# Optimization experiments

Hardware: AMD Instinct MI355X
Metric: run time of the kernel (lower is better)

The kernel has to match this reference:

```python
import jax, jax.numpy as jnp
import numpy as np
from jax import lax

T, X, H = 16384, 256, 1024
A_SCALE, A_IDENT = 0.1, 0.9


def setup_inputs() -> dict:
    key = jax.random.key(0)
    k1, k2, k3 = jax.random.split(key, 3)
    x_seq = jax.random.normal(k1, (T, X), dtype=jnp.float32)
    h0 = jnp.zeros((H,), dtype=jnp.float32)
    # orthogonal-like init for A_raw (QR of a gaussian), lecun_normal for B
    g = jax.random.normal(k2, (H, H), dtype=jnp.float32)
    A_raw, _ = jnp.linalg.qr(g)
    B = jax.random.normal(k3, (H, X), dtype=jnp.float32) * (1.0 / np.sqrt(X))
    c = jnp.zeros((H,), dtype=jnp.float32)
    return {"x_seq": x_seq, "h0": h0, "A_raw": A_raw, "B": B, "c": c}


def reference(x_seq, h0, A_raw, B, c):
    # A = a_identity * I + a_scale * A_raw  (computed in setup(), a parameter transform)
    A = A_IDENT * jnp.eye(H, dtype=x_seq.dtype) + A_SCALE * A_raw
    # Precompute input projections for all timesteps as one GEMM: (T,H)
    Bx_c = x_seq @ B.T + c  # B @ x_t + c for every t

    def step(h, bx_t):
        h_new = jnp.tanh(A @ h + bx_t)
        return h_new, h_new

    _, h_all = lax.scan(step, h0, Bx_c)
    return h_all  # (T, H)
```

## Files before the change

kernel.cpp:

```cpp
#include <hip/hip_runtime.h>
#include <cstdint>

#define T_LEN 16384
#define X_DIM 256
#define H_DIM 1024
#define NREP  8
#define SLOT_U32 1024
#define REP_U32  (2 * SLOT_U32)
#define FLAG_OFF (NREP * REP_U32)

typedef unsigned int u32;
typedef u32   u32x4 __attribute__((ext_vector_type(4)));
typedef float f32x4 __attribute__((ext_vector_type(4)));

__device__ __forceinline__ void coh_store4(u32* p, u32x4 v) {
  asm volatile("global_store_dwordx4 %0, %1, off sc0 sc1" :: "v"(p), "v"(v) : "memory");
}
__device__ __forceinline__ void coh_store1(u32* p, u32 v) {
  asm volatile("global_store_dword %0, %1, off sc0 sc1" :: "v"(p), "v"(v) : "memory");
}
__device__ __forceinline__ u32 coh_load1(const u32* p) {
  u32 v;
  asm volatile("global_load_dword %0, %1, off sc0 sc1\n\ts_waitcnt vmcnt(0)"
               : "=v"(v) : "v"(p) : "memory");
  return v;
}
__device__ __forceinline__ void poll_group(const u32* p, u32x4& a, u32x4& b,
                                           u32x4& c, u32x4& d) {
  asm volatile(
      "global_load_dwordx4 %0, %4, off sc0 sc1\n\t"
      "global_load_dwordx4 %1, %4, off offset:16 sc0 sc1\n\t"
      "global_load_dwordx4 %2, %4, off offset:32 sc0 sc1\n\t"
      "global_load_dwordx4 %3, %4, off offset:48 sc0 sc1\n\t"
      "s_waitcnt vmcnt(0)"
      : "=&v"(a), "=&v"(b), "=&v"(c), "=&v"(d) : "v"(p) : "memory");
}

__device__ __forceinline__ float fast_tanh(float x) {
  x = fminf(9.0f, fmaxf(-9.0f, x));
  const float e = __builtin_amdgcn_exp2f(x * 2.8853900817779268f);
  return (e - 1.0f) * __builtin_amdgcn_rcpf(e + 1.0f);
}

template <int CTRL>
__device__ __forceinline__ float ror_add(float x) {
  const int y = __builtin_amdgcn_update_dpp(0, __float_as_int(x), CTRL, 0xF, 0xF, false);
  return x + __int_as_float(y);
}
__device__ __forceinline__ float redux64(float x) {
  x = ror_add<0x121>(x);
  x = ror_add<0x122>(x);
  x = ror_add<0x124>(x);
  x = ror_add<0x128>(x);
  x += __shfl_xor(x, 16, 64);
  x += __shfl_xor(x, 32, 64);
  return x;
}

__global__ void hinit(const float* __restrict__ h0, u32* __restrict__ ws) {
  const int i = threadIdx.x;
  const f32x4 h = *(const f32x4*)(h0 + i * 4);
  u32x4 v;
  v.x = __float_as_uint(h[0]) & ~3u;
  v.y = __float_as_uint(h[1]) & ~3u;
  v.z = __float_as_uint(h[2]) & ~3u;
  v.w = __float_as_uint(h[3]) & ~3u;
  const int idx = i * 4;
#pragma unroll
  for (int rep = 0; rep < NREP; ++rep)
    coh_store4(ws + (size_t)rep * REP_U32 + idx, v);
  if (i < 2) coh_store1(ws + FLAG_OFF + i, 0u);
}

__global__ __launch_bounds__(256) void gemm_bx(const float* __restrict__ x,
                                               const float* __restrict__ Bm,
                                               const float* __restrict__ c,
                                               float* __restrict__ out) {
  __shared__ float xs[64][68];
  __shared__ float bs[64][68];

  const int tid = threadIdx.x;
  const int t0  = blockIdx.x * 64;
  const int h0  = blockIdx.y * 64;
  const int lr  = tid >> 4;
  const int lc  = tid & 15;

  float acc[4][4] = {};

  for (int kb = 0; kb < X_DIM; kb += 64) {
    const int kk  = (tid & 15) * 4;
    const int tt0 = tid >> 4;
#pragma unroll
    for (int i = 0; i < 4; ++i) {
      const int tt = tt0 + i * 16;
      const f32x4 xv = *(const f32x4*)(x  + (size_t)(t0 + tt) * X_DIM + kb + kk);
      const f32x4 bv = *(const f32x4*)(Bm + (size_t)(h0 + tt) * X_DIM + kb + kk);
#pragma unroll
      for (int q = 0; q < 4; ++q) {
        xs[kk + q][tt] = xv[q];
        bs[kk + q][tt] = bv[q];
      }
    }
    __syncthreads();

#pragma unroll 8
    for (int k = 0; k < 64; ++k) {
      const f32x4 xv = *(const f32x4*)&xs[k][lr * 4];
      const f32x4 bv = *(const f32x4*)&bs[k][lc * 4];
#pragma unroll
      for (int i = 0; i < 4; ++i)
#pragma unroll
        for (int j = 0; j < 4; ++j)
          acc[i][j] = fmaf(xv[i], bv[j], acc[i][j]);
    }
    __syncthreads();
  }

  const f32x4 cv = *(const f32x4*)(c + h0 + lc * 4);
#pragma unroll
  for (int i = 0; i < 4; ++i) {
    f32x4 o;
#pragma unroll
    for (int j = 0; j < 4; ++j) o[j] = acc[i][j] + cv[j];
    *(f32x4*)(out + (size_t)(t0 + lr * 4 + i) * H_DIM + h0 + lc * 4) = o;
  }
}

__global__ __launch_bounds__(256) void rnn_scan(const float* __restrict__ A_raw,
                                                float* __restrict__ out,
                                                u32* __restrict__ ws) {
  const int tid = threadIdx.x;

  if (blockIdx.x >= 64) {
    const u32* flag = ws + FLAG_OFF;
    float f0 = 0.f, f1 = 0.f, f2 = 0.f, f3 = 0.f;
    float f4 = 0.f, f5 = 0.f, f6 = 0.f, f7 = 0.f;
    const float m = 1.0000001f, ad = 1e-9f;
    for (int outer = 0; outer < 32768; ++outer) {
      if (coh_load1(flag) != 0u) break;
      for (int i = 0; i < 256; ++i) {
        f0 = fmaf(f0, m, ad); f1 = fmaf(f1, m, ad);
        f2 = fmaf(f2, m, ad); f3 = fmaf(f3, m, ad);
        f4 = fmaf(f4, m, ad); f5 = fmaf(f5, m, ad);
        f6 = fmaf(f6, m, ad); f7 = fmaf(f7, m, ad);
      }
    }
    if (f0 + f1 + f2 + f3 + f4 + f5 + f6 + f7 == 123456.789f && tid == 0)
      coh_store1(ws + FLAG_OFF + 1, 1u);
    return;
  }

  const int lane    = tid & 63;
  const int wv      = tid >> 6;
  const int wg      = blockIdx.x;
  const int gw      = wg * 4 + wv;
  const int rowbase = gw * 4;
  const int r       = lane & 3;
  const int row     = rowbase + r;

  float a[4][16];
#pragma unroll
  for (int rr = 0; rr < 4; ++rr) {
#pragma unroll
    for (int k4 = 0; k4 < 4; ++k4) {
      const f32x4 v = *(const f32x4*)(A_raw + (size_t)(rowbase + rr) * H_DIM +
                                      lane * 16 + k4 * 4);
#pragma unroll
      for (int q = 0; q < 4; ++q) {
        const int col = lane * 16 + k4 * 4 + q;
        a[rr][k4 * 4 + q] = 0.1f * v[q] + (col == rowbase + rr ? 0.9f : 0.0f);
      }
    }
  }

  u32* hbuf = ws;
  const u32* ppoll0 = hbuf + (size_t)(gw & (NREP - 1)) * REP_U32 + 16 * lane;
  u32* pub = hbuf + (size_t)(lane >> 2) * REP_U32 + rowbase + r;

  float bx_val = out[(size_t)0 * H_DIM + row];
  float bx_n1  = out[(size_t)1 * H_DIM + row];

  int  dead    = 1 << 20;
  bool timeout = false;

  for (int t = 0; t < T_LEN; ++t) {
    const u32 tag = (u32)(t & 3);
    const u32* p  = ppoll0 + (t & 1) * SLOT_U32;
    u32x4 hA, hB, hC, hD;
    for (;;) {
      poll_group(p, hA, hB, hC, hD);
      const u32 m = (hA.x ^ tag) | (hA.y ^ tag) | (hA.z ^ tag) | (hA.w ^ tag)
                  | (hB.x ^ tag) | (hB.y ^ tag) | (hB.z ^ tag) | (hB.w ^ tag)
                  | (hC.x ^ tag) | (hC.y ^ tag) | (hC.z ^ tag) | (hC.w ^ tag)
                  | (hD.x ^ tag) | (hD.y ^ tag) | (hD.z ^ tag) | (hD.w ^ tag);
      if ((m & 3u) == 0u) break;
      if (--dead == 0) { timeout = true; break; }
    }
    if (__any(timeout)) {
      if (lane == 0) coh_store1(ws + FLAG_OFF, 1u);
      return;
    }

    const int tn2 = (t + 2 < T_LEN) ? t + 2 : t;
    const float bx_n2 = out[(size_t)tn2 * H_DIM + row];

    const f32x4 f0 = __builtin_bit_cast(f32x4, hA);
    const f32x4 f1 = __builtin_bit_cast(f32x4, hB);
    const f32x4 f2 = __builtin_bit_cast(f32x4, hC);
    const f32x4 f3 = __builtin_bit_cast(f32x4, hD);
    float ac0 = 0.f, ac1 = 0.f, ac2 = 0.f, ac3 = 0.f;
#pragma unroll
    for (int j = 0; j < 4; ++j) {
      ac0 = fmaf(a[0][j], f0[j], ac0); ac1 = fmaf(a[1][j], f0[j], ac1);
      ac2 = fmaf(a[2][j], f0[j], ac2); ac3 = fmaf(a[3][j], f0[j], ac3);
    }
#pragma unroll
    for (int j = 0; j < 4; ++j) {
      ac0 = fmaf(a[0][4 + j], f1[j], ac0); ac1 = fmaf(a[1][4 + j], f1[j], ac1);
      ac2 = fmaf(a[2][4 + j], f1[j], ac2); ac3 = fmaf(a[3][4 + j], f1[j], ac3);
    }
#pragma unroll
    for (int j = 0; j < 4; ++j) {
      ac0 = fmaf(a[0][8 + j], f2[j], ac0); ac1 = fmaf(a[1][8 + j], f2[j], ac1);
      ac2 = fmaf(a[2][8 + j], f2[j], ac2); ac3 = fmaf(a[3][8 + j], f2[j], ac3);
    }
#pragma unroll
    for (int j = 0; j < 4; ++j) {
      ac0 = fmaf(a[0][12 + j], f3[j], ac0); ac1 = fmaf(a[1][12 + j], f3[j], ac1);
      ac2 = fmaf(a[2][12 + j], f3[j], ac2); ac3 = fmaf(a[3][12 + j], f3[j], ac3);
    }

    ac0 = redux64(ac0);
    ac1 = redux64(ac1);
    ac2 = redux64(ac2);
    ac3 = redux64(ac3);

    float accr = ac0;
    if (r == 1) accr = ac1;
    if (r == 2) accr = ac2;
    if (r == 3) accr = ac3;
    const float v = fast_tanh(accr + bx_val);
    bx_val = bx_n1;
    bx_n1  = bx_n2;

    const u32 nt = (u32)((t + 1) & 3);
    if (lane < 4 * NREP) {
      coh_store1(pub + (size_t)((t + 1) & 1) * SLOT_U32,
                 (__float_as_uint(v) & ~3u) | nt);
    } else if (lane < 4 * NREP + 4) {
      out[(size_t)t * H_DIM + row] = v;
    }
  }

  if (gw == 0 && lane == 0) coh_store1(ws + FLAG_OFF, 1u);
}

extern "C" void kernel_launch(void* const* d_in, const int* in_sizes, int n_in,
                              void* d_out, int out_size, void* d_ws, size_t ws_size,
                              hipStream_t stream) {
  const float* x    = (const float*)d_in[0];
  const float* h0   = (const float*)d_in[1];
  const float* Araw = (const float*)d_in[2];
  const float* B    = (const float*)d_in[3];
  const float* c    = (const float*)d_in[4];
  float* out = (float*)d_out;
  u32* ws    = (u32*)d_ws;

  hinit<<<1, 256, 0, stream>>>(h0, ws);
  dim3 g(T_LEN / 64, H_DIM / 64);
  gemm_bx<<<g, 256, 0, stream>>>(x, B, c, out);
  rnn_scan<<<256, 256, 0, stream>>>(Araw, out, ws);
}
```

Before: 22.25 ms.

## Pipeline spin-wait polling with double-buffered in-flight loads in inline asm

Replaces the serial poll loop, which waited for each round of loads to finish before checking tags, with a hand-written assembly loop that keeps two sets of sentinel and data loads in flight. Lanes drop out of exec as soon as their sentinels match, and the result is taken from whichever buffer succeeded. A fallback poll loop covers the case where the full vectors do not all carry the matching tag. The aim is to cut the latency of cross-workgroup handoffs in the per-timestep recurrence, at the cost of extra memory traffic and more complex exec-mask handling.

```diff
diff --git a/kernel.cpp b/kernel.cpp
--- a/kernel.cpp
+++ b/kernel.cpp
@@ -10,6 +10,7 @@
 #define FLAG_OFF (NREP * REP_U32)
 
 typedef unsigned int u32;
+typedef unsigned long long u64;
 typedef u32   u32x4 __attribute__((ext_vector_type(4)));
 typedef float f32x4 __attribute__((ext_vector_type(4)));
 
@@ -36,6 +37,15 @@
       : "=&v"(a), "=&v"(b), "=&v"(c), "=&v"(d) : "v"(p) : "memory");
 }
 
+__device__ __forceinline__ u32 tagchk(const u32x4& a, const u32x4& b,
+                                      const u32x4& c, const u32x4& d, u32 tag) {
+  const u32 m = (a.x ^ tag) | (a.y ^ tag) | (a.z ^ tag) | (a.w ^ tag)
+              | (b.x ^ tag) | (b.y ^ tag) | (b.z ^ tag) | (b.w ^ tag)
+              | (c.x ^ tag) | (c.y ^ tag) | (c.z ^ tag) | (c.w ^ tag)
+              | (d.x ^ tag) | (d.y ^ tag) | (d.z ^ tag) | (d.w ^ tag);
+  return m & 3u;
+}
+
 __device__ __forceinline__ float fast_tanh(float x) {
   x = fminf(9.0f, fmaxf(-9.0f, x));
   const float e = __builtin_amdgcn_exp2f(x * 2.8853900817779268f);
@@ -56,6 +66,27 @@
   x += __shfl_xor(x, 32, 64);
   return x;
 }
+
+#define ISSUE_SET(s0, s1, s2, s3, f0, f1, f2, f3)                        \
+  "global_load_dword %[" #s0 "], %[gp], off sc0 sc1\n\t"                 \
+  "global_load_dword %[" #s1 "], %[gp], off offset:16 sc0 sc1\n\t"       \
+  "global_load_dword %[" #s2 "], %[gp], off offset:32 sc0 sc1\n\t"       \
+  "global_load_dword %[" #s3 "], %[gp], off offset:48 sc0 sc1\n\t"       \
+  "global_load_dwordx4 %[" #f0 "], %[gp], off sc0 sc1\n\t"               \
+  "global_load_dwordx4 %[" #f1 "], %[gp], off offset:16 sc0 sc1\n\t"     \
+  "global_load_dwordx4 %[" #f2 "], %[gp], off offset:32 sc0 sc1\n\t"     \
+  "global_load_dwordx4 %[" #f3 "], %[gp], off offset:48 sc0 sc1\n\t"
+
+#define CHK_SENT(s0, s1, s2, s3)                                         \
+  "v_xor_b32 %[t], %[stag], %[" #s0 "]\n\t"                              \
+  "v_xor_b32 %[u], %[stag], %[" #s1 "]\n\t"                              \
+  "v_or_b32 %[t], %[t], %[u]\n\t"                                        \
+  "v_xor_b32 %[u], %[stag], %[" #s2 "]\n\t"                              \
+  "v_or_b32 %[t], %[t], %[u]\n\t"                                        \
+  "v_xor_b32 %[u], %[stag], %[" #s3 "]\n\t"                              \
+  "v_or_b32 %[t], %[t], %[u]\n\t"                                        \
+  "v_and_b32 %[t], 3, %[t]\n\t"                                          \
+  "v_cmp_ne_u32 vcc, 0, %[t]\n\t"
 
 __global__ void hinit(const float* __restrict__ h0, u32* __restrict__ ws) {
   const int i = threadIdx.x;
@@ -180,25 +211,80 @@
   float bx_val = out[(size_t)0 * H_DIM + row];
   float bx_n1  = out[(size_t)1 * H_DIM + row];
 
-  int  dead    = 1 << 20;
+  int  dead2   = 1 << 20;
   bool timeout = false;
 
   for (int t = 0; t < T_LEN; ++t) {
     const u32 tag = (u32)(t & 3);
     const u32* p  = ppoll0 + (t & 1) * SLOT_U32;
-    u32x4 hA, hB, hC, hD;
-    for (;;) {
-      poll_group(p, hA, hB, hC, hD);
-      const u32 m = (hA.x ^ tag) | (hA.y ^ tag) | (hA.z ^ tag) | (hA.w ^ tag)
-                  | (hB.x ^ tag) | (hB.y ^ tag) | (hB.z ^ tag) | (hB.w ^ tag)
-                  | (hC.x ^ tag) | (hC.y ^ tag) | (hC.z ^ tag) | (hC.w ^ tag)
-                  | (hD.x ^ tag) | (hD.y ^ tag) | (hD.z ^ tag) | (hD.w ^ tag);
-      if ((m & 3u) == 0u) break;
-      if (--dead == 0) { timeout = true; break; }
-    }
-    if (__any(timeout)) {
+
+    u32x4 fa0, fa1, fa2, fa3, fb0, fb1, fb2, fb3;
+    u32 sa0, sa1, sa2, sa3, sb0, sb1, sb2, sb3;
+    u32 tmp1, tmp2, wh, tmo, sdead;
+    u64 sv, sm, st;
+    asm volatile(
+        "s_waitcnt vmcnt(0)\n\t"
+        "s_mov_b64 %[sv], exec\n\t"
+        "s_mov_b32 %[sd], 0x200000\n\t"
+        "v_mov_b32 %[wh], 0\n\t"
+        "v_mov_b32 %[to], 0\n\t"
+        ISSUE_SET(xa0, xa1, xa2, xa3, qa0, qa1, qa2, qa3)
+        ISSUE_SET(xb0, xb1, xb2, xb3, qb0, qb1, qb2, qb3)
+        "Lp%=:\n\t"
+        "s_waitcnt vmcnt(8)\n\t"
+        CHK_SENT(xa0, xa1, xa2, xa3)
+        "s_and_b64 exec, exec, vcc\n\t"
+        "s_cbranch_execz Ld%=\n\t"
+        "s_sub_u32 %[sd], %[sd], 1\n\t"
+        "s_cbranch_scc1 Lt%=\n\t"
+        ISSUE_SET(xa0, xa1, xa2, xa3, qa0, qa1, qa2, qa3)
+        "s_waitcnt vmcnt(8)\n\t"
+        CHK_SENT(xb0, xb1, xb2, xb3)
+        "s_andn2_b64 %[sm], exec, vcc\n\t"
+        "s_mov_b64 %[st], exec\n\t"
+        "s_mov_b64 exec, %[sm]\n\t"
+        "v_mov_b32 %[wh], 1\n\t"
+        "s_mov_b64 exec, %[st]\n\t"
+        "s_and_b64 exec, exec, vcc\n\t"
+        "s_cbranch_execz Ld%=\n\t"
+        "s_sub_u32 %[sd], %[sd], 1\n\t"
+        "s_cbranch_scc1 Lt%=\n\t"
+        ISSUE_SET(xb0, xb1, xb2, xb3, qb0, qb1, qb2, qb3)
+        "s_branch Lp%=\n\t"
+        "Lt%=:\n\t"
+        "v_mov_b32 %[to], 1\n\t"
+        "Ld%=:\n\t"
+        "s_waitcnt vmcnt(0)\n\t"
+        "s_mov_b64 exec, %[sv]\n\t"
+        : [qa0]"=&v"(fa0), [qa1]"=&v"(fa1), [qa2]"=&v"(fa2), [qa3]"=&v"(fa3),
+          [qb0]"=&v"(fb0), [qb1]"=&v"(fb1), [qb2]"=&v"(fb2), [qb3]"=&v"(fb3),
+          [xa0]"=&v"(sa0), [xa1]"=&v"(sa1), [xa2]"=&v"(sa2), [xa3]"=&v"(sa3),
+          [xb0]"=&v"(sb0), [xb1]"=&v"(sb1), [xb2]"=&v"(sb2), [xb3]"=&v"(sb3),
+          [t]"=&v"(tmp1), [u]"=&v"(tmp2), [wh]"=&v"(wh), [to]"=&v"(tmo),
+          [sd]"=&s"(sdead), [sv]"=&s"(sv), [sm]"=&s"(sm), [st]"=&s"(st)
+        : [gp]"v"(p), [stag]"s"(tag)
+        : "vcc", "scc", "memory");
+
+    if (__any(tmo != 0u)) {
       if (lane == 0) coh_store1(ws + FLAG_OFF, 1u);
       return;
+    }
+
+    u32x4 hA = wh ? fb0 : fa0;
+    u32x4 hB = wh ? fb1 : fa1;
+    u32x4 hC = wh ? fb2 : fa2;
+    u32x4 hD = wh ? fb3 : fa3;
+
+    if (__any(tagchk(hA, hB, hC, hD, tag) != 0u)) {
+      for (;;) {
+        poll_group(p, hA, hB, hC, hD);
+        if (tagchk(hA, hB, hC, hD, tag) == 0u) break;
+        if (--dead2 == 0) { timeout = true; break; }
+      }
+      if (__any(timeout)) {
+        if (lane == 0) coh_store1(ws + FLAG_OFF, 1u);
+        return;
+      }
     }
 
     const int tn2 = (t + 2 < T_LEN) ? t + 2 : t;
```

Result: slower. 63.55 ms (+185.6%).
